# Performance work log

Measured on AMD Instinct MI355X. Metric: run time of the kernel, lower is better.

The kernel has to match this reference:

```python
import jax, jax.numpy as jnp
from jax import lax
import numpy as np

WS = 8        # window size
SHIFT = 4     # shift size
HEADS = 4
EPS = 1e-5


def _rel_pos_index(ws):
    coords = np.stack(np.meshgrid(np.arange(ws), np.arange(ws), indexing='ij'))  # (2,ws,ws)
    cf = coords.reshape(2, -1)
    rel = cf[:, :, None] - cf[:, None, :]           # (2,n,n)
    rel = rel.transpose(1, 2, 0).astype(np.int64)   # (n,n,2)
    rel[:, :, 0] += ws - 1
    rel[:, :, 1] += ws - 1
    rel[:, :, 0] *= 2 * ws - 1
    return rel.sum(-1)                              # (n,n)


def _attn_mask(h, w, ws, ss):
    img = np.zeros((h, w), dtype=np.float32)
    cnt = 0
    for hs in (slice(0, -ws), slice(-ws, -ss), slice(-ss, None)):
        for wsl in (slice(0, -ws), slice(-ws, -ss), slice(-ss, None)):
            img[hs, wsl] = cnt
            cnt += 1
    mw = img.reshape(h // ws, ws, w // ws, ws).transpose(0, 2, 1, 3).reshape(-1, ws * ws)
    am = mw[:, None, :] - mw[:, :, None]            # (nW,n,n)
    return np.where(am != 0, -100.0, 0.0).astype(np.float32)


def _ln(x, w, b):
    mu = x.mean(-1, keepdims=True)
    var = jnp.var(x, axis=-1, keepdims=True)
    return (x - mu) * lax.rsqrt(var + EPS) * w + b


def setup_inputs() -> dict:
    key = jax.random.key(0)
    ks = jax.random.split(key, 16)
    b, c, h, w = 4, 64, 256, 256
    hidden = 4 * c
    n_bias = (2 * WS - 1) * (2 * WS - 1)
    s = 0.02
    return {
        'x': jax.random.normal(ks[0], (b, c, h, w), jnp.float32),
        'norm1_w': jnp.ones((c,), jnp.float32),
        'norm1_b': jnp.zeros((c,), jnp.float32),
        'qkv_w': jax.random.normal(ks[1], (3 * c, c), jnp.float32) * s,
        'qkv_b': jnp.zeros((3 * c,), jnp.float32),
        'rpb': jax.random.normal(ks[2], (n_bias, HEADS), jnp.float32) * s,
        'proj_w': jax.random.normal(ks[3], (c, c), jnp.float32) * s,
        'proj_b': jnp.zeros((c,), jnp.float32),
        'norm2_w': jnp.ones((c,), jnp.float32),
        'norm2_b': jnp.zeros((c,), jnp.float32),
        'fc1_w': jax.random.normal(ks[4], (hidden, c), jnp.float32) * s,
        'fc1_b': jnp.zeros((hidden,), jnp.float32),
        'dw_w': jax.random.normal(ks[5], (hidden, 1, 5, 5), jnp.float32) * s,
        'dw_b': jnp.zeros((hidden,), jnp.float32),
        'fc2_w': jax.random.normal(ks[6], (c, hidden), jnp.float32) * s,
        'fc2_b': jnp.zeros((c,), jnp.float32),
    }


def reference(x, norm1_w, norm1_b, qkv_w, qkv_b, rpb, proj_w, proj_b,
              norm2_w, norm2_b, fc1_w, fc1_b, dw_w, dw_b, fc2_w, fc2_b):
    b, c, h, w = x.shape
    d = c // HEADS
    scale = d ** (-0.5)
    n = WS * WS

    x3 = jnp.transpose(x.reshape(b, c, h * w), (0, 2, 1))  # (b, hw, c)
    shortcut = x3
    xn = _ln(x3, norm1_w, norm1_b).reshape(b, h, w, c)

    # cyclic shift + window partition
    sx = jnp.roll(xn, (-SHIFT, -SHIFT), axis=(1, 2))
    win = sx.reshape(b, h // WS, WS, w // WS, WS, c).transpose(0, 1, 3, 2, 4, 5).reshape(-1, n, c)
    B_ = win.shape[0]

    qkv = (win @ qkv_w.T + qkv_b).reshape(B_, n, 3, HEADS, d).transpose(2, 0, 3, 1, 4)
    q, k, v = qkv[0] * scale, qkv[1], qkv[2]   # (B_, H, n, d)
    attn = jnp.einsum('bhnd,bhmd->bhnm', q, k)  # (B_, H, n, n)

    bias = rpb[jnp.asarray(_rel_pos_index(WS)).reshape(-1)].reshape(n, n, HEADS).transpose(2, 0, 1)
    attn = attn + bias[None]

    mask = jnp.asarray(_attn_mask(h, w, WS, SHIFT))  # (nW, n, n)
    nW = mask.shape[0]
    attn = attn.reshape(B_ // nW, nW, HEADS, n, n) + mask[None, :, None]
    attn = jax.nn.softmax(attn.reshape(B_, HEADS, n, n), axis=-1)

    out = jnp.einsum('bhnm,bhmd->bhnd', attn, v).transpose(0, 2, 1, 3).reshape(B_, n, c)
    out = out @ proj_w.T + proj_b

    # window reverse + un-shift
    sx = out.reshape(b, h // WS, w // WS, WS, WS, c).transpose(0, 1, 3, 2, 4, 5).reshape(b, h, w, c)
    xr = jnp.roll(sx, (SHIFT, SHIFT), axis=(1, 2)).reshape(b, h * w, c)
    x3 = shortcut + xr

    # ConvFFN
    xn = _ln(x3, norm2_w, norm2_b)
    hid = jax.nn.gelu(xn @ fc1_w.T + fc1_b, approximate=False)  # (b, hw, hidden)
    hidden = hid.shape[-1]
    himg = hid.transpose(0, 2, 1).reshape(b, hidden, h, w)
    dc = lax.conv_general_dilated(himg, dw_w, (1, 1), [(2, 2), (2, 2)],
                                  dimension_numbers=('NCHW', 'OIHW', 'NCHW'),
                                  feature_group_count=hidden)
    dc = jax.nn.gelu(dc + dw_b[None, :, None, None], approximate=False)
    hid = hid + dc.reshape(b, hidden, h * w).transpose(0, 2, 1)
    x3 = x3 + (hid @ fc2_w.T + fc2_b)

    return jnp.transpose(x3, (0, 2, 1)).reshape(b, c, h, w)
```

## Files before the change

kernel.cpp:

```cpp
#include <hip/hip_runtime.h>
#include <hip/hip_bf16.h>
#include <hip/hip_fp8.h>
#include <math.h>


typedef __bf16  bf16x8  __attribute__((ext_vector_type(8)));
typedef float   f32x4   __attribute__((ext_vector_type(4)));
typedef float   f32x2   __attribute__((ext_vector_type(2)));
typedef unsigned short ushortx8 __attribute__((ext_vector_type(8)));

__device__ __forceinline__ float gelu_f(float v) {
    float u = v * fmaf(0.0713548354f, v * v, 1.5957691216f);
    float t = __expf(u);
    float r = __builtin_amdgcn_rcpf(t + 1.0f);
    return v - v * r;
}
__device__ __forceinline__ unsigned char f32_to_fp8(float v) {
    __hip_fp8_e4m3 t(v);
    return (unsigned char)t.__x;
}
__device__ __forceinline__ float fp8_to_f32(unsigned char u) {
    __hip_fp8_e4m3 t;
    t.__x = (__hip_fp8_storage_t)u;
    return (float)t;
}

#if __has_builtin(__builtin_amdgcn_cvt_pk_f32_fp8) && __has_builtin(__builtin_amdgcn_cvt_pk_fp8_f32)
#define HW_FP8 1
#endif
template<bool HI>
__device__ __forceinline__ f32x2 fp8x2_f32(unsigned int u) {
#ifdef HW_FP8
    return __builtin_amdgcn_cvt_pk_f32_fp8((int)u, HI);
#else
    f32x2 r;
    const int s = HI ? 16 : 0;
    r.x = fp8_to_f32((unsigned char)(u >> s));
    r.y = fp8_to_f32((unsigned char)(u >> (s + 8)));
    return r;
#endif
}
template<bool HI>
__device__ __forceinline__ unsigned int f32x2_fp8(float a, float b, unsigned int old) {
#ifdef HW_FP8
    return (unsigned int)__builtin_amdgcn_cvt_pk_fp8_f32(a, b, (int)old, HI);
#else
    unsigned int v = (unsigned int)f32_to_fp8(a) | ((unsigned int)f32_to_fp8(b) << 8);
    return HI ? ((old & 0x0000ffffu) | (v << 16)) : ((old & 0xffff0000u) | v);
#endif
}

__device__ __forceinline__ unsigned short f2bf(float f) {
    unsigned int u = __builtin_bit_cast(unsigned int, f);
    u += 0x7fffu + ((u >> 16) & 1u);
    return (unsigned short)(u >> 16);
}
__device__ __forceinline__ float bf2f(unsigned short u) {
    return __builtin_bit_cast(float, ((unsigned int)u) << 16);
}
__device__ __forceinline__ unsigned int cvt_pk_bf16(float a, float b) {
#if defined(__gfx950__)
    unsigned int r;
    asm("v_cvt_pk_bf16_f32 %0, %1, %2" : "=v"(r) : "v"(a), "v"(b));
    return r;
#else
    return (unsigned int)f2bf(a) | ((unsigned int)f2bf(b) << 16);
#endif
}

__global__ __launch_bounds__(256) void k_prep(
        const float* __restrict__ qkvw, const float* __restrict__ projw,
        const float* __restrict__ rpb,  const float* __restrict__ fc1w,
        unsigned short* __restrict__ qkvw_bf, unsigned short* __restrict__ projw_bf,
        unsigned short* __restrict__ rpb_bf,  unsigned short* __restrict__ fc1w_bf) {
    const int i = blockIdx.x * 256 + threadIdx.x;
    if (i < 12288) qkvw_bf[i] = f2bf(qkvw[i]);
    if (i < 4096)  projw_bf[i] = f2bf(projw[i]);
    if (i < 900)   rpb_bf[i]   = f2bf(rpb[i]);
    if (i < 16384) fc1w_bf[i]  = f2bf(fc1w[i]);
}

__global__ __launch_bounds__(256) void k_cvt(const float* __restrict__ src,
        unsigned short* __restrict__ dst, int n) {
    const int i = blockIdx.x * 256 + threadIdx.x;
    if (i < n) dst[i] = f2bf(src[i]);
}

__global__ __launch_bounds__(256) void k_ln1(const float* __restrict__ x,
        const float* __restrict__ w1, const float* __restrict__ b1,
        unsigned short* __restrict__ A, unsigned short* __restrict__ Bw) {
    __shared__ float tile[64 * 65];
    __shared__ float red0[256], red1[256];
    __shared__ float muv[64], rsv[64], lw[64], lb[64];
    const int tid = threadIdx.x;
    const int gid = blockIdx.x;
    const int xc = gid & 3, y = (gid >> 2) & 255, b = gid >> 10;
    const int x0 = xc * 64;
    if (tid < 64) { lw[tid] = w1[tid]; lb[tid] = b1[tid]; }

    const float* xb = x + ((size_t)b * 64) * 65536 + y * 256 + x0;
    {
        const int tk = tid & 63, cl = tid >> 6;
        for (int it = 0; it < 16; ++it) {
            int cc = cl + 4 * it;
            tile[cc * 65 + tk] = xb[(size_t)cc * 65536 + tk];
        }
    }
    __syncthreads();
    {
        const int tk = tid & 63, cl = tid >> 6;
        float s = 0.f, s2 = 0.f;
        #pragma unroll
        for (int k = 0; k < 16; ++k) {
            float v = tile[(cl * 16 + k) * 65 + tk];
            s += v; s2 += v * v;
        }
        red0[cl * 64 + tk] = s; red1[cl * 64 + tk] = s2;
    }
    __syncthreads();
    if (tid < 64) {
        float s  = red0[tid] + red0[64 + tid] + red0[128 + tid] + red0[192 + tid];
        float s2 = red1[tid] + red1[64 + tid] + red1[128 + tid] + red1[192 + tid];
        float mu = s * (1.f / 64.f);
        float var = s2 * (1.f / 64.f) - mu * mu;
        muv[tid] = mu; rsv[tid] = rsqrtf(var + 1e-5f);
    }
    __syncthreads();
    const int ch = tid & 63, tl = tid >> 6;
    const int ys = (y + 252) & 255;
    const int wy = ys >> 3, py = ys & 7;
    for (int it = 0; it < 16; ++it) {
        int t = tl + 4 * it;
        float v = tile[ch * 65 + t];
        int tok = (b << 16) + y * 256 + x0 + t;
        A[(size_t)tok * 64 + ch] = f2bf(v);
        float vn = (v - muv[t]) * rsv[t] * lw[ch] + lb[ch];
        int xs = (x0 + t + 252) & 255;
        int wx = xs >> 3, px = xs & 7;
        int widx = (b << 10) + (wy << 5) + wx;
        int pos = (py << 3) + px;
        Bw[((size_t)widx * 64 + pos) * 64 + ch] = f2bf(vn);
    }
}

__global__ __launch_bounds__(256) void k_attn(
        const unsigned short* __restrict__ Bw,
        const unsigned short* __restrict__ qkvw_bf,
        const unsigned short* __restrict__ projw_bf,
        const unsigned short* __restrict__ rpb_bf,
        const float* __restrict__ qkvb,
        const float* __restrict__ projb,
        const unsigned short* __restrict__ A, unsigned short* __restrict__ Cb) {
    __shared__ __align__(16) unsigned short Xs[4608];
    __shared__ __align__(16) unsigned short Ws[13824];
    __shared__ __align__(8)  unsigned short rpbl[900];
    __shared__ float qkvbl[192];
    __shared__ float projbl[64];

    const int tid = threadIdx.x;
    const int lane = tid & 63, wv = tid >> 6;
    const int l15 = lane & 15, quad = lane >> 4;
    const int widx = blockIdx.x;
    const int wib = widx & 1023;
    const int wy = wib >> 5, wx = wib & 31, bimg = widx >> 10;
    const bool edge = (wy == 31) | (wx == 31);

    const f32x4 zz = {0.f, 0.f, 0.f, 0.f};
    const ushortx8 zu = {0, 0, 0, 0, 0, 0, 0, 0};
    const bf16x8 z8 = __builtin_bit_cast(bf16x8, zu);
    const ushortx8 ou = {0x3F80, 0x3F80, 0x3F80, 0x3F80, 0x3F80, 0x3F80, 0x3F80, 0x3F80};
    const bf16x8 ones8 = __builtin_bit_cast(bf16x8, ou);

    const ushortx8 pw0 = *(const ushortx8*)(projw_bf + tid * 8);
    const ushortx8 pw1 = *(const ushortx8*)(projw_bf + (256 + tid) * 8);

    {
        const unsigned short* Xg = Bw + (size_t)widx * 4096 + wv * 1024;
        #pragma unroll
        for (int it = 0; it < 2; ++it) {
            int g = it * 64 + lane;
            int row = g >> 3, c8 = g & 7;
            *(ushortx8*)&Xs[(wv * 16 + row) * 72 + c8 * 8] =
                *(const ushortx8*)(Xg + g * 8);
        }
    }
    #pragma unroll
    for (int it = 0; it < 6; ++it) {
        int g = it * 256 + tid;
        int row = g >> 3, c8 = g & 7;
        *(ushortx8*)&Ws[row * 72 + c8 * 8] = *(const ushortx8*)(qkvw_bf + g * 8);
    }
    if (tid < 225) *(uint2*)&rpbl[tid * 4] = *(const uint2*)(rpb_bf + tid * 4);
    if (tid < 192) qkvbl[tid] = qkvb[tid];
    if (tid < 64)  projbl[tid] = projb[tid];
    __syncthreads();

    f32x4 qacc[12];
    #pragma unroll
    for (int i = 0; i < 12; ++i) qacc[i] = zz;
    {
        const bf16x8 av0 = *(const bf16x8*)&Xs[(16 * wv + l15) * 72 + quad * 8];
        const bf16x8 av1 = *(const bf16x8*)&Xs[(16 * wv + l15) * 72 + 32 + quad * 8];
        #pragma unroll
        for (int gl = 0; gl < 12; ++gl) {
            bf16x8 bv0 = *(const bf16x8*)&Ws[(gl * 16 + l15) * 72 + quad * 8];
            qacc[gl] = __builtin_amdgcn_mfma_f32_16x16x32_bf16(av0, bv0, qacc[gl], 0, 0, 0);
            bf16x8 bv1 = *(const bf16x8*)&Ws[(gl * 16 + l15) * 72 + 32 + quad * 8];
            qacc[gl] = __builtin_amdgcn_mfma_f32_16x16x32_bf16(av1, bv1, qacc[gl], 0, 0, 0);
        }
    }
    __syncthreads();

    #pragma unroll
    for (int g = 0; g < 12; ++g) {
        #pragma unroll
        for (int r = 0; r < 4; ++r) {
            int tok = 16 * wv + quad * 4 + r;
            int oc  = g * 16 + l15;
            float v = qacc[g][r] + qkvbl[oc];
            if (g < 4)       Ws[g * 1024 + tok * 16 + l15] = f2bf(v * 0.25f);
            else if (g < 8)  Ws[4096 + (g - 4) * 1024 + tok * 16 + l15] = f2bf(v);
            else             Ws[8192 + ((g - 8) * 16 + l15) * 72 + tok] = f2bf(v);
        }
    }
    __syncthreads();

    f32x4 sacc[4][4];
    #pragma unroll
    for (int h = 0; h < 4; ++h) {
        bf16x8 qa = z8;
        if (quad < 2) qa = *(const bf16x8*)&Ws[h * 1024 + (16 * wv + l15) * 16 + quad * 8];
        #pragma unroll
        for (int nt = 0; nt < 4; ++nt) {
            bf16x8 kf = z8;
            if (quad < 2) kf = *(const bf16x8*)&Ws[4096 + h * 1024 + (nt * 16 + l15) * 16 + quad * 8];
            sacc[h][nt] = __builtin_amdgcn_mfma_f32_16x16x32_bf16(qa, kf, zz, 0, 0, 0);
        }
    }
    __syncthreads();

    {
        const int r0 = tid >> 3;
        *(ushortx8*)&Ws[4096 + r0 * 64 + (((tid & 7) ^ (r0 & 7)) << 3)] = pw0;
        const int g1 = 256 + tid, r1 = g1 >> 3;
        *(ushortx8*)&Ws[4096 + r1 * 64 + (((g1 & 7) ^ (r1 & 7)) << 3)] = pw1;
    }

    const int jhi = l15 >> 3, jlo = l15 & 7;
    int offj4[4], regj[4];
    #pragma unroll
    for (int nt = 0; nt < 4; ++nt) {
        int j = nt * 16 + l15;
        int jy = j >> 3, jx = j & 7;
        offj4[nt] = (jy * 15 + jx) * 4;
        regj[nt] = 0;
        if (edge) {
            int ysj = wy * 8 + jy, xsj = wx * 8 + jx;
            regj[nt] = (ysj >= 252 ? 2 : (ysj >= 248 ? 1 : 0)) * 3
                     + (xsj >= 252 ? 2 : (xsj >= 248 ? 1 : 0));
        }
    }
    int rbA[4], regiA[4], pbaseA[4], i7A[4];
    #pragma unroll
    for (int r = 0; r < 4; ++r) {
        const int i = 16 * wv + quad * 4 + r;
        const int iy = i >> 3, ix = i & 7;
        rbA[r] = ((iy + 7) * 15 + (ix + 7)) * 4;
        i7A[r] = i & 7;
        pbaseA[r] = i * 64 + jlo;
        regiA[r] = 0;
        if (edge) {
            const int ysi = wy * 8 + iy, xsi = wx * 8 + ix;
            regiA[r] = (ysi >= 252 ? 2 : (ysi >= 248 ? 1 : 0)) * 3
                     + (xsi >= 252 ? 2 : (xsi >= 248 ? 1 : 0));
        }
    }

    #pragma unroll
    for (int r = 0; r < 4; ++r) {
        #pragma unroll
        for (int nt = 0; nt < 4; ++nt) {
            const uint2 bw = *(const uint2*)&rpbl[rbA[r] - offj4[nt]];
            float mk = 0.f;
            if (edge) mk = (regj[nt] == regiA[r]) ? 0.f : -100.f;
            sacc[0][nt][r] += __builtin_bit_cast(float, bw.x << 16) + mk;
            sacc[1][nt][r] += __builtin_bit_cast(float, bw.x & 0xffff0000u) + mk;
            sacc[2][nt][r] += __builtin_bit_cast(float, bw.y << 16) + mk;
            sacc[3][nt][r] += __builtin_bit_cast(float, bw.y & 0xffff0000u) + mk;
        }
    }
    int pA_[4][4];
    #pragma unroll
    for (int r = 0; r < 4; ++r)
        #pragma unroll
        for (int nt = 0; nt < 4; ++nt)
            pA_[r][nt] = pbaseA[r] + ((((nt << 1) | jhi) ^ i7A[r]) << 3);

    f32x4 o[4];
    #pragma unroll
    for (int h = 0; h < 4; ++h) {
        #pragma unroll
        for (int r = 0; r < 4; ++r) {
            const unsigned int pk01 = cvt_pk_bf16(__expf(sacc[h][0][r]),
                                                  __expf(sacc[h][1][r]));
            const unsigned int pk23 = cvt_pk_bf16(__expf(sacc[h][2][r]),
                                                  __expf(sacc[h][3][r]));
            Ws[pA_[r][0]] = (unsigned short)pk01;
            Ws[pA_[r][1]] = (unsigned short)(pk01 >> 16);
            Ws[pA_[r][2]] = (unsigned short)pk23;
            Ws[pA_[r][3]] = (unsigned short)(pk23 >> 16);
        }
        o[h] = zz;
        f32x4 os = zz;
        #pragma unroll
        for (int s = 0; s < 2; ++s) {
            bf16x8 pa = *(const bf16x8*)&Ws[(16 * wv + l15) * 64
                                            + (((s * 4 + quad) ^ (l15 & 7)) << 3)];
            bf16x8 vb = *(const bf16x8*)&Ws[8192 + (h * 16 + l15) * 72 + s * 32 + quad * 8];
            o[h] = __builtin_amdgcn_mfma_f32_16x16x32_bf16(pa, vb, o[h], 0, 0, 0);
            os   = __builtin_amdgcn_mfma_f32_16x16x32_bf16(pa, ones8, os, 0, 0, 0);
        }
        #pragma unroll
        for (int r = 0; r < 4; ++r) o[h][r] *= __builtin_amdgcn_rcpf(os[r]);
    }

    unsigned short resid[16];
    #pragma unroll
    for (int r = 0; r < 4; ++r) {
        int tok = 16 * wv + quad * 4 + r;
        int py = tok >> 3, px = tok & 7;
        int yo = (wy * 8 + py + 4) & 255, xo = (wx * 8 + px + 4) & 255;
        size_t gt = ((size_t)bimg << 16) + yo * 256 + xo;
        #pragma unroll
        for (int nt = 0; nt < 4; ++nt)
            resid[r * 4 + nt] = A[gt * 64 + nt * 16 + l15];
    }

    #pragma unroll
    for (int h = 0; h < 4; ++h)
        #pragma unroll
        for (int r = 0; r < 4; ++r)
            Xs[(16 * wv + quad * 4 + r) * 72 + h * 16 + l15] = f2bf(o[h][r]);
    __syncthreads();

    f32x4 pacc[4];
    #pragma unroll
    for (int nt = 0; nt < 4; ++nt) {
        pacc[nt] = zz;
        #pragma unroll
        for (int s = 0; s < 2; ++s) {
            bf16x8 oa = *(const bf16x8*)&Xs[(16 * wv + l15) * 72 + s * 32 + quad * 8];
            bf16x8 wb = *(const bf16x8*)&Ws[4096 + (nt * 16 + l15) * 64
                                            + (((s * 4 + quad) ^ (l15 & 7)) << 3)];
            pacc[nt] = __builtin_amdgcn_mfma_f32_16x16x32_bf16(oa, wb, pacc[nt], 0, 0, 0);
        }
    }

    #pragma unroll
    for (int r = 0; r < 4; ++r) {
        int tok = 16 * wv + quad * 4 + r;
        int py = tok >> 3, px = tok & 7;
        int yo = (wy * 8 + py + 4) & 255, xo = (wx * 8 + px + 4) & 255;
        size_t gt = ((size_t)bimg << 16) + yo * 256 + xo;
        #pragma unroll
        for (int nt = 0; nt < 4; ++nt) {
            int oc = nt * 16 + l15;
            float v = pacc[nt][r] + projbl[oc] + bf2f(resid[r * 4 + nt]);
            Cb[gt * 64 + oc] = f2bf(v);
        }
    }
}

__global__ __launch_bounds__(256) void k_ln2fc1(const unsigned short* __restrict__ Cb,
        const float* __restrict__ w2, const float* __restrict__ b2,
        const unsigned short* __restrict__ fc1w_bf, const float* __restrict__ fc1b,
        unsigned char* __restrict__ D) {
    __shared__ __align__(16) unsigned short Xb[64 * 72];
    __shared__ __align__(16) unsigned short Wb[256 * 72];
    __shared__ float red0[256], red1[256];
    __shared__ float muv[64], rsv[64], lwv[64], lbv[64], fb[256];
    const int tid = threadIdx.x, gid = blockIdx.x;
    const int xc = gid & 3, y = (gid >> 2) & 255, b = gid >> 10;
    const int x0 = xc * 64;
    const int lane = tid & 63, wv = tid >> 6;
    const int l15 = lane & 15, quad = lane >> 4;
    const f32x4 zz = {0.f, 0.f, 0.f, 0.f};

    if (tid < 64) { lwv[tid] = w2[tid]; lbv[tid] = b2[tid]; }
    fb[tid] = fc1b[tid];

    const unsigned short* Cp = Cb + ((size_t)(b << 16) + y * 256 + x0) * 64;
    #pragma unroll
    for (int it = 0; it < 16; ++it) {
        int tt = wv + 4 * it;
        Xb[tt * 72 + lane] = Cp[tt * 64 + lane];
    }
    {
        const ushortx8* w8 = (const ushortx8*)fc1w_bf;
        #pragma unroll
        for (int it = 0; it < 8; ++it) {
            int idx = it * 256 + tid;
            int row = idx >> 3, c8 = idx & 7;
            *(ushortx8*)&Wb[row * 72 + c8 * 8] = w8[idx];
        }
    }
    __syncthreads();
    {
        const int tok = tid & 63, cl = tid >> 6;
        float s = 0.f, s2 = 0.f;
        #pragma unroll
        for (int g = 0; g < 2; ++g) {
            const ushortx8 u = *(const ushortx8*)&Xb[tok * 72 + cl * 16 + g * 8];
            #pragma unroll
            for (int k = 0; k < 8; ++k) { float v = bf2f(u[k]); s += v; s2 += v * v; }
        }
        red0[cl * 64 + tok] = s; red1[cl * 64 + tok] = s2;
    }
    __syncthreads();
    if (tid < 64) {
        float s  = red0[tid] + red0[64 + tid] + red0[128 + tid] + red0[192 + tid];
        float s2 = red1[tid] + red1[64 + tid] + red1[128 + tid] + red1[192 + tid];
        float mu = s * (1.f / 64.f);
        float var = s2 * (1.f / 64.f) - mu * mu;
        muv[tid] = mu; rsv[tid] = rsqrtf(var + 1e-5f);
    }
    __syncthreads();
    #pragma unroll
    for (int it = 0; it < 16; ++it) {
        int tt = wv + 4 * it;
        float v = bf2f(Xb[tt * 72 + lane]);
        v = (v - muv[tt]) * rsv[tt] * lwv[lane] + lbv[lane];
        Xb[tt * 72 + lane] = f2bf(v);
    }
    __syncthreads();

    f32x4 acc[4][4];
    #pragma unroll
    for (int mt = 0; mt < 4; ++mt)
        #pragma unroll
        for (int nt = 0; nt < 4; ++nt) acc[mt][nt] = zz;
    #pragma unroll
    for (int s = 0; s < 2; ++s) {
        bf16x8 Bf[4];
        #pragma unroll
        for (int nt = 0; nt < 4; ++nt)
            Bf[nt] = *(const bf16x8*)&Xb[(nt * 16 + l15) * 72 + s * 32 + quad * 8];
        #pragma unroll
        for (int mt = 0; mt < 4; ++mt) {
            bf16x8 Af = *(const bf16x8*)&Wb[(64 * wv + 16 * mt + l15) * 72 + s * 32 + quad * 8];
            #pragma unroll
            for (int nt = 0; nt < 4; ++nt)
                acc[mt][nt] = __builtin_amdgcn_mfma_f32_16x16x32_bf16(Af, Bf[nt], acc[mt][nt], 0, 0, 0);
        }
    }

    #pragma unroll
    for (int mt = 0; mt < 4; ++mt) {
        #pragma unroll
        for (int r = 0; r < 4; ++r) {
            const int mch = 64 * wv + 16 * mt + quad * 4 + r;
            const float bias = fb[mch];
            unsigned char* Dp = D + (((size_t)(b * 256 + mch)) << 16) + y * 256 + x0;
            float g0 = gelu_f(acc[mt][0][r] + bias);
            float g1 = gelu_f(acc[mt][1][r] + bias);
            float g2 = gelu_f(acc[mt][2][r] + bias);
            float g3 = gelu_f(acc[mt][3][r] + bias);
            unsigned int pk = f32x2_fp8<false>(g0, g1, 0u);
            pk = f32x2_fp8<true>(g2, g3, pk);
            Dp[l15]      = (unsigned char)(pk);
            Dp[16 + l15] = (unsigned char)(pk >> 8);
            Dp[32 + l15] = (unsigned char)(pk >> 16);
            Dp[48 + l15] = (unsigned char)(pk >> 24);
        }
    }
}

__global__ __launch_bounds__(256) void k_dwconv(const unsigned char* __restrict__ D,
        const float* __restrict__ dww, const float* __restrict__ dwb,
        unsigned char* __restrict__ E) {
    __shared__ __align__(16) unsigned short inT[36 * 280 + 16];
    __shared__ __align__(16) unsigned short Atab[5 * 64 * 8];
    __shared__ __align__(16) unsigned char outT[4][16 * 144];
    const int tid = threadIdx.x, gid = blockIdx.x;
    const int yt = gid & 7, pc = gid >> 3;
    const int ch = pc & 255;
    const int y0 = yt * 32;
    const unsigned char* Dp = D + ((size_t)pc << 16);
    const f32x4 zz = {0.f, 0.f, 0.f, 0.f};

    #pragma unroll
    for (int it = 0; it < 5; ++it) {
        int idx = it * 256 + tid;
        if (idx < 1262) ((uint4*)inT)[idx] = make_uint4(0, 0, 0, 0);
    }
    __syncthreads();

    #pragma unroll
    for (int it = 0; it < 9; ++it) {
        const int u = it * 256 + tid;
        const int t = u >> 6, c = u & 63;
        const int gy = y0 - 2 + t;
        if ((unsigned)gy < 256u) {
            const unsigned int v = *(const unsigned int*)(Dp + gy * 256 + 4 * c);
            const f32x2 lo = fp8x2_f32<false>(v);
            const f32x2 hi = fp8x2_f32<true>(v);
            unsigned int b01 = (unsigned)f2bf(lo.x) | ((unsigned)f2bf(lo.y) << 16);
            unsigned int b23 = (unsigned)f2bf(hi.x) | ((unsigned)f2bf(hi.y) << 16);
            unsigned int* base = (unsigned int*)&inT[t * 280 + 2 + 4 * c];
            base[0] = b01; base[1] = b23;
        }
    }
    #pragma unroll
    for (int q = 0; q < 10; ++q) {
        const int e = tid * 10 + q;
        const int ky = e >> 9, r = e & 511;
        const int l = r >> 3, j = r & 7;
        const int m = l & 15, k = ((l >> 4) << 3) + j;
        const int d = k - m;
        float wv = 0.f;
        if (d >= 0 && d < 5) wv = dww[ch * 25 + ky * 5 + d];
        Atab[e] = f2bf(wv);
    }
    const float bb = dwb[ch];
    __syncthreads();

    const int wv_ = tid >> 6, lane = tid & 63;
    const int l15 = lane & 15, quad = lane >> 4;
    const int g = wv_ >> 1, xh = wv_ & 1;
    bf16x8 Af[5];
    #pragma unroll
    for (int ky = 0; ky < 5; ++ky)
        Af[ky] = *(const bf16x8*)&Atab[(ky * 64 + lane) * 8];
    const int tbase = g * 16 + l15;

    #pragma unroll
    for (int xp = 0; xp < 8; ++xp) {
        const int xs = xh * 128 + xp * 16;
        f32x4 acc = zz;
        #pragma unroll
        for (int ky = 0; ky < 5; ++ky) {
            bf16x8 Bf = *(const bf16x8*)&inT[(tbase + ky) * 280 + xs + quad * 8];
            acc = __builtin_amdgcn_mfma_f32_16x16x32_bf16(Af[ky], Bf, acc, 0, 0, 0);
        }
        const unsigned int* cp32 = (const unsigned int*)&inT[(tbase + 2) * 280 + 2 + xs + quad * 4];
        const unsigned int c01 = cp32[0], c23 = cp32[1];
        const float c0 = bf2f((unsigned short)c01), c1 = bf2f((unsigned short)(c01 >> 16));
        const float c2 = bf2f((unsigned short)c23), c3 = bf2f((unsigned short)(c23 >> 16));
        unsigned int pk = f32x2_fp8<false>(c0 + gelu_f(acc[0] + bb), c1 + gelu_f(acc[1] + bb), 0u);
        pk = f32x2_fp8<true>(c2 + gelu_f(acc[2] + bb), c3 + gelu_f(acc[3] + bb), pk);
        *(unsigned int*)&outT[wv_][l15 * 144 + xp * 16 + quad * 4] = pk;
    }

    {
        const int row = lane >> 2, sg = lane & 3;
        unsigned char* Ep = E + ((size_t)pc << 16) + (y0 + g * 16 + row) * 256 + xh * 128 + sg * 32;
        *(uint4*)Ep        = *(const uint4*)&outT[wv_][row * 144 + sg * 32];
        *(uint4*)(Ep + 16) = *(const uint4*)&outT[wv_][row * 144 + sg * 32 + 16];
    }
}

__global__ __launch_bounds__(256) void k_fc2(const unsigned char* __restrict__ E,
        const unsigned short* __restrict__ Cb, const unsigned short* __restrict__ fc2w_bf,
        const float* __restrict__ fc2b, float* __restrict__ out) {
    __shared__ __align__(16) unsigned short Hb[64 * 136];
    __shared__ __align__(16) unsigned short Wb2[64 * 264];
    __shared__ __align__(16) unsigned short Cl[64 * 72];
    __shared__ float fbl[64];
    const int tid = threadIdx.x, gid = blockIdx.x;
    const int xc = gid & 3, y = (gid >> 2) & 255, b = gid >> 10;
    const int x0 = xc * 64;
    const int lane = tid & 63, wv = tid >> 6;
    const int l15 = lane & 15, quad = lane >> 4;
    const f32x4 zz = {0.f, 0.f, 0.f, 0.f};

    if (tid < 64) fbl[tid] = fc2b[tid];
    {
        const unsigned short* Cp = Cb + ((size_t)(b << 16) + y * 256 + x0) * 64;
        #pragma unroll
        for (int it = 0; it < 16; ++it) {
            int tt = wv + 4 * it;
            Cl[tt * 72 + lane] = Cp[tt * 64 + lane];
        }
    }
    {
        const ushortx8* w8 = (const ushortx8*)fc2w_bf;
        #pragma unroll
        for (int it = 0; it < 8; ++it) {
            int idx = it * 256 + tid;
            int row = idx >> 5, c8 = idx & 31;
            *(ushortx8*)&Wb2[row * 264 + c8 * 8] = w8[idx];
        }
    }

    f32x4 acc[4];
    #pragma unroll
    for (int nt = 0; nt < 4; ++nt) acc[nt] = zz;

    const int ldc = tid >> 4;
    const int tq  = tid & 15;
    unsigned int u0[8];
    #pragma unroll
    for (int it = 0; it < 8; ++it) {
        int chl = ldc + 16 * it;
        u0[it] = *(const unsigned int*)&E[(((size_t)(b * 256 + chl)) << 16) + y * 256 + x0 + 4 * tq];
    }
    __syncthreads();

    for (int kc = 0; kc < 2; ++kc) {
        #pragma unroll
        for (int it = 0; it < 8; ++it) {
            int chl = ldc + 16 * it;
            f32x2 lo = fp8x2_f32<false>(u0[it]);
            f32x2 hi = fp8x2_f32<true>(u0[it]);
            float vals[4] = {lo.x, lo.y, hi.x, hi.y};
            #pragma unroll
            for (int j = 0; j < 4; ++j) {
                int tok = 4 * tq + j;
                int p = (((chl >> 3) ^ (tok >> 2)) << 3) + (chl & 7);
                Hb[tok * 136 + p] = f2bf(vals[j]);
            }
        }
        if (kc == 0) {
            #pragma unroll
            for (int it = 0; it < 8; ++it) {
                int chl = ldc + 16 * it + 128;
                u0[it] = *(const unsigned int*)&E[(((size_t)(b * 256 + chl)) << 16) + y * 256 + x0 + 4 * tq];
            }
        }
        __syncthreads();
        #pragma unroll
        for (int k32 = 0; k32 < 4; ++k32) {
            bf16x8 Af = *(const bf16x8*)&Wb2[(16 * wv + l15) * 264 + kc * 128 + k32 * 32 + quad * 8];
            const int g = k32 * 4 + quad;
            #pragma unroll
            for (int nt = 0; nt < 4; ++nt) {
                const int tok = nt * 16 + l15;
                bf16x8 Bf = *(const bf16x8*)&Hb[tok * 136 + ((g ^ (tok >> 2)) << 3)];
                acc[nt] = __builtin_amdgcn_mfma_f32_16x16x32_bf16(Af, Bf, acc[nt], 0, 0, 0);
            }
        }
        if (kc == 0) __syncthreads();
    }

    #pragma unroll
    for (int r = 0; r < 4; ++r) {
        const int oc = 16 * wv + quad * 4 + r;
        const float bias = fbl[oc];
        float* op = out + (((size_t)(b * 64 + oc)) << 16) + y * 256 + x0;
        #pragma unroll
        for (int nt = 0; nt < 4; ++nt) {
            const int tok = nt * 16 + l15;
            op[tok] = acc[nt][r] + bias + bf2f(Cl[tok * 72 + oc]);
        }
    }
}

extern "C" void kernel_launch(void* const* d_in, const int* in_sizes, int n_in,
                              void* d_out, int out_size, void* d_ws, size_t ws_size,
                              hipStream_t stream) {
    const float* x     = (const float*)d_in[0];
    const float* n1w   = (const float*)d_in[1];
    const float* n1b   = (const float*)d_in[2];
    const float* qkvw  = (const float*)d_in[3];
    const float* qkvb  = (const float*)d_in[4];
    const float* rpb   = (const float*)d_in[5];
    const float* projw = (const float*)d_in[6];
    const float* projb = (const float*)d_in[7];
    const float* n2w   = (const float*)d_in[8];
    const float* n2b   = (const float*)d_in[9];
    const float* fc1w  = (const float*)d_in[10];
    const float* fc1b  = (const float*)d_in[11];
    const float* dww   = (const float*)d_in[12];
    const float* dwb   = (const float*)d_in[13];
    const float* fc2w  = (const float*)d_in[14];
    const float* fc2b  = (const float*)d_in[15];
    float* out = (float*)d_out;

    char* ws = (char*)d_ws;
    const size_t MB = 1048576;
    unsigned short* Cbuf = (unsigned short*)ws;
    unsigned short* Ab   = (unsigned short*)(ws + 32 * MB);
    unsigned short* Bwp  = (unsigned short*)(ws + 64 * MB);
    unsigned char*  Dh   = (unsigned char*)(ws + 32 * MB);
    unsigned char*  Eh   = (unsigned char*)(ws + 96 * MB);

    unsigned short* qkvw_bf = (unsigned short*)(ws + 96 * MB);
    unsigned short* projw_bf = (unsigned short*)(ws + 96 * MB + 24576);
    unsigned short* rpb_bf   = (unsigned short*)(ws + 96 * MB + 32768);
    unsigned short* fc1w_bf  = (unsigned short*)(ws + 96 * MB + 34816);
    unsigned short* fc2w_bf  = (unsigned short*)(ws + 32 * MB);

    k_prep  <<<64,    256, 0, stream>>>(qkvw, projw, rpb, fc1w,
                                        qkvw_bf, projw_bf, rpb_bf, fc1w_bf);
    k_ln1   <<<4096,  256, 0, stream>>>(x, n1w, n1b, Ab, Bwp);
    k_attn  <<<4096,  256, 0, stream>>>(Bwp, qkvw_bf, projw_bf, rpb_bf,
                                        qkvb, projb, Ab, Cbuf);
    k_ln2fc1<<<4096,  256, 0, stream>>>(Cbuf, n2w, n2b, fc1w_bf, fc1b, Dh);
    k_dwconv<<<8192,  256, 0, stream>>>(Dh, dww, dwb, Eh);
    k_cvt   <<<64,    256, 0, stream>>>(fc2w, fc2w_bf, 16384);
    k_fc2   <<<4096,  256, 0, stream>>>(Eh, Cbuf, fc2w_bf, fc2b, out);
}
```

Before: 361.7 us.

## Vectorize global/LDS accesses and bf16 packing across LN, fc1, dwconv, fc2 kernels

Across several kernels, scalar 16-bit and byte stores and loads become wider ones. The LN/window-partition kernel writes packed bf16 pairs. The fc1 and fc2 kernels load the residual tile with 16-byte vectors, and the fc1 LayerNorm pass works on 8 channels per thread. The fc1 epilogue stages fp8 results through LDS (reusing the weight buffer) so each lane writes 4-byte words instead of single bytes. The dwconv kernel zeroes only the halo columns and drops a barrier, and bf16 conversion uses a packed convert helper. The aim is fewer memory transactions, at the cost of extra LDS traffic and relying on the weight buffer no longer being read when it is reused.

```diff
diff --git a/kernel.cpp b/kernel.cpp
--- a/kernel.cpp
+++ b/kernel.cpp
@@ -126,20 +126,27 @@
         muv[tid] = mu; rsv[tid] = rsqrtf(var + 1e-5f);
     }
     __syncthreads();
-    const int ch = tid & 63, tl = tid >> 6;
+    const int cp = tid & 31, ch0 = cp * 2;
+    const int tl = tid >> 5;
+    const float2 lwp = *(const float2*)&lw[ch0];
+    const float2 lbp = *(const float2*)&lb[ch0];
     const int ys = (y + 252) & 255;
     const int wy = ys >> 3, py = ys & 7;
-    for (int it = 0; it < 16; ++it) {
-        int t = tl + 4 * it;
-        float v = tile[ch * 65 + t];
-        int tok = (b << 16) + y * 256 + x0 + t;
-        A[(size_t)tok * 64 + ch] = f2bf(v);
-        float vn = (v - muv[t]) * rsv[t] * lw[ch] + lb[ch];
-        int xs = (x0 + t + 252) & 255;
-        int wx = xs >> 3, px = xs & 7;
-        int widx = (b << 10) + (wy << 5) + wx;
-        int pos = (py << 3) + px;
-        Bw[((size_t)widx * 64 + pos) * 64 + ch] = f2bf(vn);
+    #pragma unroll
+    for (int it = 0; it < 8; ++it) {
+        const int t = tl + 8 * it;
+        const float v0 = tile[ch0 * 65 + t];
+        const float v1 = tile[(ch0 + 1) * 65 + t];
+        const int tok = (b << 16) + y * 256 + x0 + t;
+        *(unsigned int*)&A[(size_t)tok * 64 + ch0] = cvt_pk_bf16(v0, v1);
+        const float mu = muv[t], rs = rsv[t];
+        const float vn0 = (v0 - mu) * rs * lwp.x + lbp.x;
+        const float vn1 = (v1 - mu) * rs * lwp.y + lbp.y;
+        const int xs = (x0 + t + 252) & 255;
+        const int wx = xs >> 3, px = xs & 7;
+        const int widx = (b << 10) + (wy << 5) + wx;
+        const int pos = (py << 3) + px;
+        *(unsigned int*)&Bw[((size_t)widx * 64 + pos) * 64 + ch0] = cvt_pk_bf16(vn0, vn1);
     }
 }
 
@@ -391,9 +398,10 @@
 
     const unsigned short* Cp = Cb + ((size_t)(b << 16) + y * 256 + x0) * 64;
     #pragma unroll
-    for (int it = 0; it < 16; ++it) {
-        int tt = wv + 4 * it;
-        Xb[tt * 72 + lane] = Cp[tt * 64 + lane];
+    for (int it = 0; it < 2; ++it) {
+        const int g = it * 256 + tid;
+        const int row = g >> 3, c8 = g & 7;
+        *(ushortx8*)&Xb[row * 72 + c8 * 8] = *(const ushortx8*)(Cp + g * 8);
     }
     {
         const ushortx8* w8 = (const ushortx8*)fc1w_bf;
@@ -425,12 +433,27 @@
         muv[tid] = mu; rsv[tid] = rsqrtf(var + 1e-5f);
     }
     __syncthreads();
-    #pragma unroll
-    for (int it = 0; it < 16; ++it) {
-        int tt = wv + 4 * it;
-        float v = bf2f(Xb[tt * 72 + lane]);
-        v = (v - muv[tt]) * rsv[tt] * lwv[lane] + lbv[lane];
-        Xb[tt * 72 + lane] = f2bf(v);
+    {
+        const int c8n = tid & 7;
+        const float4 lwa = *(const float4*)&lwv[c8n * 8];
+        const float4 lwb2 = *(const float4*)&lwv[c8n * 8 + 4];
+        const float4 lba = *(const float4*)&lbv[c8n * 8];
+        const float4 lbb2 = *(const float4*)&lbv[c8n * 8 + 4];
+        const float lw8[8] = {lwa.x, lwa.y, lwa.z, lwa.w, lwb2.x, lwb2.y, lwb2.z, lwb2.w};
+        const float lb8[8] = {lba.x, lba.y, lba.z, lba.w, lbb2.x, lbb2.y, lbb2.z, lbb2.w};
+        #pragma unroll
+        for (int it = 0; it < 2; ++it) {
+            const int row = it * 32 + (tid >> 3);
+            const ushortx8 u = *(const ushortx8*)&Xb[row * 72 + c8n * 8];
+            const float mu = muv[row], rs = rsv[row];
+            float v[8];
+            #pragma unroll
+            for (int k = 0; k < 8; ++k) v[k] = (bf2f(u[k]) - mu) * rs * lw8[k] + lb8[k];
+            uint4 pk;
+            pk.x = cvt_pk_bf16(v[0], v[1]); pk.y = cvt_pk_bf16(v[2], v[3]);
+            pk.z = cvt_pk_bf16(v[4], v[5]); pk.w = cvt_pk_bf16(v[6], v[7]);
+            *(uint4*)&Xb[row * 72 + c8n * 8] = pk;
+        }
     }
     __syncthreads();
 
@@ -454,23 +477,33 @@
         }
     }
 
+    unsigned int* stT = (unsigned int*)&Wb[(size_t)(64 * wv) * 72];
+    const int s4 = lane >> 4;
     #pragma unroll
     for (int mt = 0; mt < 4; ++mt) {
         #pragma unroll
         for (int r = 0; r < 4; ++r) {
             const int mch = 64 * wv + 16 * mt + quad * 4 + r;
             const float bias = fb[mch];
-            unsigned char* Dp = D + (((size_t)(b * 256 + mch)) << 16) + y * 256 + x0;
             float g0 = gelu_f(acc[mt][0][r] + bias);
             float g1 = gelu_f(acc[mt][1][r] + bias);
             float g2 = gelu_f(acc[mt][2][r] + bias);
             float g3 = gelu_f(acc[mt][3][r] + bias);
             unsigned int pk = f32x2_fp8<false>(g0, g1, 0u);
             pk = f32x2_fp8<true>(g2, g3, pk);
-            Dp[l15]      = (unsigned char)(pk);
-            Dp[16 + l15] = (unsigned char)(pk >> 8);
-            Dp[32 + l15] = (unsigned char)(pk >> 16);
-            Dp[48 + l15] = (unsigned char)(pk >> 24);
+            stT[(quad * 4 + r) * 20 + l15] = pk;
+        }
+        const int orow = l15;
+        const uint4 w = *(const uint4*)&stT[orow * 20 + 4 * s4];
+        const int mch2 = 64 * wv + 16 * mt + orow;
+        unsigned char* Dp2 = D + (((size_t)(b * 256 + mch2)) << 16) + y * 256 + x0;
+        #pragma unroll
+        for (int p = 0; p < 4; ++p) {
+            unsigned int o = ((w.x >> (8 * p)) & 0xffu)
+                           | (((w.y >> (8 * p)) & 0xffu) << 8)
+                           | (((w.z >> (8 * p)) & 0xffu) << 16)
+                           | (((w.w >> (8 * p)) & 0xffu) << 24);
+            *(unsigned int*)&Dp2[16 * p + 4 * s4] = o;
         }
     }
 }
@@ -488,27 +521,23 @@
     const unsigned char* Dp = D + ((size_t)pc << 16);
     const f32x4 zz = {0.f, 0.f, 0.f, 0.f};
 
-    #pragma unroll
-    for (int it = 0; it < 5; ++it) {
-        int idx = it * 256 + tid;
-        if (idx < 1262) ((uint4*)inT)[idx] = make_uint4(0, 0, 0, 0);
-    }
-    __syncthreads();
-
+    for (int idx = tid; idx < 432; idx += 256) {
+        const int r = idx / 12, c = idx - r * 12;
+        const int dw = (c == 0) ? 0 : (128 + c);
+        ((unsigned int*)&inT[r * 280])[dw] = 0u;
+    }
     #pragma unroll
     for (int it = 0; it < 9; ++it) {
         const int u = it * 256 + tid;
         const int t = u >> 6, c = u & 63;
         const int gy = y0 - 2 + t;
-        if ((unsigned)gy < 256u) {
-            const unsigned int v = *(const unsigned int*)(Dp + gy * 256 + 4 * c);
-            const f32x2 lo = fp8x2_f32<false>(v);
-            const f32x2 hi = fp8x2_f32<true>(v);
-            unsigned int b01 = (unsigned)f2bf(lo.x) | ((unsigned)f2bf(lo.y) << 16);
-            unsigned int b23 = (unsigned)f2bf(hi.x) | ((unsigned)f2bf(hi.y) << 16);
-            unsigned int* base = (unsigned int*)&inT[t * 280 + 2 + 4 * c];
-            base[0] = b01; base[1] = b23;
-        }
+        unsigned int v = 0u;
+        if ((unsigned)gy < 256u) v = *(const unsigned int*)(Dp + gy * 256 + 4 * c);
+        const f32x2 lo = fp8x2_f32<false>(v);
+        const f32x2 hi = fp8x2_f32<true>(v);
+        unsigned int* base = (unsigned int*)&inT[t * 280 + 2 + 4 * c];
+        base[0] = cvt_pk_bf16(lo.x, lo.y);
+        base[1] = cvt_pk_bf16(hi.x, hi.y);
     }
     #pragma unroll
     for (int q = 0; q < 10; ++q) {
@@ -577,9 +606,10 @@
     {
         const unsigned short* Cp = Cb + ((size_t)(b << 16) + y * 256 + x0) * 64;
         #pragma unroll
-        for (int it = 0; it < 16; ++it) {
-            int tt = wv + 4 * it;
-            Cl[tt * 72 + lane] = Cp[tt * 64 + lane];
+        for (int it = 0; it < 2; ++it) {
+            const int g = it * 256 + tid;
+            const int row = g >> 3, c8 = g & 7;
+            *(ushortx8*)&Cl[row * 72 + c8 * 8] = *(const ushortx8*)(Cp + g * 8);
         }
     }
     {
@@ -612,12 +642,15 @@
             int chl = ldc + 16 * it;
             f32x2 lo = fp8x2_f32<false>(u0[it]);
             f32x2 hi = fp8x2_f32<true>(u0[it]);
-            float vals[4] = {lo.x, lo.y, hi.x, hi.y};
+            const unsigned int p01 = cvt_pk_bf16(lo.x, lo.y);
+            const unsigned int p23 = cvt_pk_bf16(hi.x, hi.y);
+            unsigned short hs[4] = {(unsigned short)p01, (unsigned short)(p01 >> 16),
+                                    (unsigned short)p23, (unsigned short)(p23 >> 16)};
             #pragma unroll
             for (int j = 0; j < 4; ++j) {
                 int tok = 4 * tq + j;
                 int p = (((chl >> 3) ^ (tok >> 2)) << 3) + (chl & 7);
-                Hb[tok * 136 + p] = f2bf(vals[j]);
+                Hb[tok * 136 + p] = hs[j];
             }
         }
         if (kc == 0) {
```

Result: no change. 360.1 us (-0.4%).
